# Optimization experiments

Hardware: AMD Instinct MI355X
Metric: run time of the kernel (lower is better)

The kernel has to match this reference:

```python
import jax, jax.numpy as jnp
import numpy as np

B, L, D, H = 2, 2048, 1024, 16
Dh = D // H

def setup_inputs() -> dict:
    key = jax.random.key(0)
    kx, kq, kk, kv, ko = jax.random.split(key, 5)
    scale = 1.0 / np.sqrt(D)
    return {
        "x": jax.random.normal(kx, (B, L, D), dtype=jnp.float32),
        "Wq": jax.random.normal(kq, (D, H, Dh), dtype=jnp.float32) * scale,
        "Wk": jax.random.normal(kk, (D, H, Dh), dtype=jnp.float32) * scale,
        "Wv": jax.random.normal(kv, (D, H, Dh), dtype=jnp.float32) * scale,
        "Wout": jax.random.normal(ko, (H, Dh, D), dtype=jnp.float32) * (1.0 / np.sqrt(D)),
    }

def reference(x, Wq, Wk, Wv, Wout):
    # QKV projections: [B,L,D] x [D,H,Dh] -> [B,L,H,Dh]
    q = jnp.einsum('bld,dhe->blhe', x, Wq)
    k = jnp.einsum('bld,dhe->blhe', x, Wk)
    v = jnp.einsum('bld,dhe->blhe', x, Wv)
    # scores [B,H,L,L]
    a = jnp.einsum('bqhd,bkhd->bhqk', q, k) / (Dh ** 0.5)
    Lq = x.shape[1]
    mask = jnp.tril(jnp.ones((1, 1, Lq, Lq), dtype=jnp.bool_))
    NEG_INF = jnp.finfo(jnp.float32).min
    a = jnp.where(mask, a, NEG_INF)
    a = jax.nn.softmax(a, axis=-1)
    o = jnp.einsum('bhqk,bkhd->bqhd', a, v)
    # output projection: [B,L,H,Dh] x [H,Dh,D] -> [B,L,D]
    return jnp.einsum('blhe,hed->bld', o, Wout)
```

## Files before the change

kernel.cpp:

```cpp
#include <hip/hip_runtime.h>

typedef __bf16 bf16x8 __attribute__((ext_vector_type(8)));
typedef __bf16 bf16x4 __attribute__((ext_vector_type(4)));
typedef float  floatx4 __attribute__((ext_vector_type(4)));
typedef float  floatx16 __attribute__((ext_vector_type(16)));

constexpr int Bc = 2, Lc = 2048, Dc = 1024, Hc = 16, Dhc = 64;
constexpr int Mr = 4096;

__device__ __forceinline__ void gl_lds16(const void* g, void* l) {
  __builtin_amdgcn_global_load_lds(
      (const __attribute__((address_space(1))) void*)g,
      (__attribute__((address_space(3))) void*)l, 16, 0, 0);
}

__global__ __launch_bounds__(256) void k_pack(const float* __restrict__ X,
                                              const float* __restrict__ W0,
                                              const float* __restrict__ W1,
                                              const float* __restrict__ W2,
                                              const float* __restrict__ W3,
                                              __bf16* __restrict__ Pw,
                                              __bf16* __restrict__ Px) {
  __shared__ __align__(16) __bf16 tile[64][66];
  int bid = blockIdx.x;
  int t = threadIdx.x;
  if (bid < 1024) {
    int z = bid >> 8, rem = bid & 255;
    int k0 = (rem & 15) << 6, n0 = (rem >> 4) << 6;
    const float* W = (z == 0) ? W0 : (z == 1) ? W1 : (z == 2) ? W2 : W3;
    __bf16* P = Pw + (size_t)z * 1024 * 1024;
    int r = t >> 2, cc = t & 3;
    const float4* src = (const float4*)&W[(size_t)(k0 + r) * 1024 + n0 + cc * 16];
#pragma unroll
    for (int i = 0; i < 4; i++) {
      float4 v = src[i];
      tile[r][cc * 16 + i * 4 + 0] = (__bf16)v.x;
      tile[r][cc * 16 + i * 4 + 1] = (__bf16)v.y;
      tile[r][cc * 16 + i * 4 + 2] = (__bf16)v.z;
      tile[r][cc * 16 + i * 4 + 3] = (__bf16)v.w;
    }
    __syncthreads();
#pragma unroll
    for (int i = 0; i < 2; i++) {
      int c = t + i * 256;
      int pl = c >> 6, nl = c & 63;
      bf16x8 o;
#pragma unroll
      for (int j = 0; j < 8; j++) o[j] = tile[pl * 8 + j][nl];
      *(bf16x8*)&P[((size_t)(k0 / 8 + pl) * 1024 + n0 + nl) * 8] = o;
    }
  } else {
    int xid = bid - 1024;
    int m0 = (xid & 63) << 6, p0 = (xid >> 6) << 2;
    int r = t >> 2, cc = t & 3;
    const float4* src = (const float4*)&X[(size_t)(m0 + r) * 1024 + p0 * 8 + cc * 8];
    float4 v0 = src[0], v1 = src[1];
    bf16x8 o;
    o[0] = (__bf16)v0.x; o[1] = (__bf16)v0.y; o[2] = (__bf16)v0.z; o[3] = (__bf16)v0.w;
    o[4] = (__bf16)v1.x; o[5] = (__bf16)v1.y; o[6] = (__bf16)v1.z; o[7] = (__bf16)v1.w;
    *(bf16x8*)&tile[0][r * 32 + cc * 8] = o;
    __syncthreads();
    int pc = t >> 6, ml = t & 63;
    bf16x8 q = *(bf16x8*)&tile[0][ml * 32 + pc * 8];
    *(bf16x8*)&Px[((size_t)(p0 + pc) * Mr + m0 + ml) * 8] = q;
  }
}

__global__ __launch_bounds__(256) void k_gemm_qkv(const __bf16* __restrict__ Ap8,
                                                  const __bf16* __restrict__ Bp8,
                                                  __bf16* __restrict__ Qb,
                                                  __bf16* __restrict__ Kb,
                                                  __bf16* __restrict__ Vb) {
  constexpr int KCB = 2080;
  constexpr int HB = 4 * KCB;
  __shared__ __align__(16) char smem[4 * HB];
  int t = threadIdx.x, lane = t & 63, w = t >> 6;
  int lh = lane >> 5, l32 = lane & 31;
  int m0 = blockIdx.x * 128;
  int mat = blockIdx.y >> 3;
  const __bf16* Bbase = Bp8 + (size_t)mat * 1024 * 1024;
  int n0loc = (blockIdx.y & 7) * 128;
  int wm = (w & 1) * 64, wn = (w >> 1) * 64;
  floatx16 acc[2][2] = {};

  auto issue = [&](int it, char* buf) {
    int kp = it << 2;
    const __bf16* ga = Ap8 + ((size_t)(kp + w) * Mr + m0 + lane) * 8;
    const __bf16* gb = Bbase + ((size_t)(kp + w) * 1024 + n0loc + lane) * 8;
    char* la = buf + w * KCB;
    char* lb = buf + HB + w * KCB;
    gl_lds16(ga, la);
    gl_lds16(ga + 512, la + 1024);
    gl_lds16(gb, lb);
    gl_lds16(gb + 512, lb + 1024);
  };

  issue(0, smem);
  for (int it = 0; it < 32; it++) {
    char* cur = smem + (it & 1) * (2 * HB);
    char* nxt = smem + ((it & 1) ^ 1) * (2 * HB);
    __syncthreads();
    if (it < 31) issue(it + 1, nxt);
    bf16x8 af[2][2], bfv[2][2];
#pragma unroll
    for (int s = 0; s < 2; s++) {
#pragma unroll
      for (int mt = 0; mt < 2; mt++)
        af[s][mt] = *(const bf16x8*)(cur + (2 * s + lh) * KCB + (wm + mt * 32 + l32) * 16);
#pragma unroll
      for (int nt = 0; nt < 2; nt++)
        bfv[s][nt] = *(const bf16x8*)(cur + HB + (2 * s + lh) * KCB + (wn + nt * 32 + l32) * 16);
    }
#pragma unroll
    for (int s = 0; s < 2; s++)
#pragma unroll
      for (int mt = 0; mt < 2; mt++)
#pragma unroll
        for (int nt = 0; nt < 2; nt++)
          acc[mt][nt] = __builtin_amdgcn_mfma_f32_32x32x16_bf16(af[s][mt], bfv[s][nt], acc[mt][nt], 0, 0, 0);
  }

  __syncthreads();

  __bf16* sl = (__bf16*)(smem + w * HB);
  int b = (m0 + wm) >> 11;
  int lbase = (m0 + wm) & 2047;
  int h = (n0loc + wn) >> 6;
  int bh2 = b * 16 + h;
  __bf16* dst;
  float scl = 1.0f;
  if (mat == 0) {
    dst = Qb + (((size_t)(bh2 * 64 + (lbase >> 5)) * 4) << 9);
    scl = 0.18033688011112042f;
  } else if (mat == 1) {
    dst = Kb + (((size_t)(bh2 * 32 + (lbase >> 6)) * 8) << 9);
  } else {
    dst = Vb + (((size_t)(bh2 * 32 + (lbase >> 6)) * 8) << 9);
  }
#pragma unroll
  for (int mt = 0; mt < 2; mt++)
#pragma unroll
    for (int nt = 0; nt < 2; nt++)
#pragma unroll
      for (int reg = 0; reg < 16; reg++) {
        int l_loc = mt * 32 + (reg & 3) + ((reg >> 2) << 3) + (lh << 2);
        int e = nt * 32 + l32;
        int off;
        if (mat == 0)
          off = ((l_loc >> 5) * 4 + ((l_loc >> 4) & 1) * 2 + (e >> 5)) * 512 +
                (((e >> 3) & 3) * 16 + (l_loc & 15)) * 8 + (e & 7);
        else if (mat == 1)
          off = ((l_loc >> 4) * 2 + (e >> 5)) * 512 +
                (((e >> 3) & 3) * 16 + (l_loc & 15)) * 8 + (e & 7);
        else
          off = ((e >> 4) * 2 + (l_loc >> 5)) * 512 +
                (((l_loc >> 2) & 3) * 16 + (e & 15)) * 8 + ((l_loc >> 4) & 1) * 4 + (l_loc & 3);
        sl[off] = (__bf16)(acc[mt][nt][reg] * scl);
      }
  __builtin_amdgcn_s_waitcnt(0);
#pragma unroll
  for (int i = 0; i < 8; i++) {
    int c = i * 64 + lane;
    bf16x8 v = *(bf16x8*)(sl + c * 8);
    *(bf16x8*)(dst + c * 8) = v;
  }
}

__global__ __launch_bounds__(256) void k_gemm_out(const __bf16* __restrict__ Ap8,
                                                  const __bf16* __restrict__ Bp8,
                                                  float* __restrict__ outF) {
  constexpr int KCB_A = 2080;
  constexpr int KCB_B = 1056;
  constexpr int BUF = 4 * KCB_A + 4 * KCB_B;
  __shared__ __align__(16) char smem[33792];
  int t = threadIdx.x, lane = t & 63, w = t >> 6;
  int lh = lane >> 5, l32 = lane & 31;
  int m0 = blockIdx.x * 128, n0 = blockIdx.y * 64;
  int wm = w * 32;
  floatx16 acc[2] = {};

  auto issue = [&](int it, char* buf) {
    int kp = it << 2;
    const __bf16* ga = Ap8 + ((size_t)(kp + w) * Mr + m0 + lane) * 8;
    const __bf16* gb = Bp8 + ((size_t)(kp + w) * 1024 + n0 + lane) * 8;
    char* la = buf + w * KCB_A;
    char* lb = buf + 4 * KCB_A + w * KCB_B;
    gl_lds16(ga, la);
    gl_lds16(ga + 512, la + 1024);
    gl_lds16(gb, lb);
  };

  issue(0, smem);
  for (int it = 0; it < 32; it++) {
    char* cur = smem + (it & 1) * BUF;
    char* nxt = smem + ((it & 1) ^ 1) * BUF;
    __syncthreads();
    if (it < 31) issue(it + 1, nxt);
    bf16x8 af[2], bfv[2][2];
#pragma unroll
    for (int s = 0; s < 2; s++) {
      af[s] = *(const bf16x8*)(cur + (2 * s + lh) * KCB_A + (wm + l32) * 16);
#pragma unroll
      for (int nt = 0; nt < 2; nt++)
        bfv[s][nt] = *(const bf16x8*)(cur + 4 * KCB_A + (2 * s + lh) * KCB_B + (nt * 32 + l32) * 16);
    }
#pragma unroll
    for (int s = 0; s < 2; s++)
#pragma unroll
      for (int nt = 0; nt < 2; nt++)
        acc[nt] = __builtin_amdgcn_mfma_f32_32x32x16_bf16(af[s], bfv[s][nt], acc[nt], 0, 0, 0);
  }

  __syncthreads();
  float* slf = (float*)(smem + w * 8448);
#pragma unroll
  for (int nt = 0; nt < 2; nt++)
#pragma unroll
    for (int reg = 0; reg < 16; reg++) {
      int rrow = (reg & 3) + ((reg >> 2) << 3) + (lh << 2);
      slf[rrow * 66 + nt * 32 + l32] = acc[nt][reg];
    }
  __builtin_amdgcn_s_waitcnt(0);
#pragma unroll
  for (int i = 0; i < 8; i++) {
    int c = i * 64 + lane;
    int row = c >> 4, sub = c & 15;
    float4 v = *(float4*)(slf + row * 66 + sub * 4);
    *(float4*)&outF[(size_t)(m0 + wm + row) * 1024 + n0 + sub * 4] = v;
  }
}

__global__ __launch_bounds__(256) void k_attn(const __bf16* __restrict__ Qf,
                                              const __bf16* __restrict__ Kf,
                                              const __bf16* __restrict__ Vf,
                                              __bf16* __restrict__ Op8) {
  __shared__ __align__(16) __bf16 POt[4][32][72];
  __shared__ float Pl[4][2][16];
  int t = threadIdx.x;
  int lane = t & 63, w = t >> 6;
  int quad = lane >> 4, l16 = lane & 15;
  int bid = blockIdx.x;
  int xcd = bid & 7, g = bid >> 3;
  int bh = xcd * 4 + (g & 3);
  int qt = 63 - (g >> 2);
  int qbase = qt * 32;

  const __bf16* Qp = Qf + (((size_t)(bh * 64 + qt) * 4) << 9) + lane * 8;
  bf16x8 qf[2][2];
#pragma unroll
  for (int mi = 0; mi < 2; mi++)
#pragma unroll
    for (int kk = 0; kk < 2; kk++)
      qf[mi][kk] = *(const bf16x8*)(Qp + ((mi * 2 + kk) << 9));

  floatx4 ot[4][2] = {};
  float l_s[2] = {0.f, 0.f};

  auto do_tile = [&](int kt, bool domask) {
    int kbase = kt * 64;
    const __bf16* Kp = Kf + (((size_t)(bh * 32 + kt) * 8) << 9) + lane * 8;
    const __bf16* Vp = Vf + (((size_t)(bh * 32 + kt) * 8) << 9) + lane * 8;
    bf16x8 ka[4][2], va[4][2];
#pragma unroll
    for (int kb = 0; kb < 4; kb++)
#pragma unroll
      for (int kk = 0; kk < 2; kk++) {
        ka[kb][kk] = *(const bf16x8*)(Kp + ((kb * 2 + kk) << 9));
        va[kb][kk] = *(const bf16x8*)(Vp + ((kb * 2 + kk) << 9));
      }

    floatx4 st[4][2] = {};
#pragma unroll
    for (int kb = 0; kb < 4; kb++)
#pragma unroll
      for (int mi = 0; mi < 2; mi++) {
        st[kb][mi] = __builtin_amdgcn_mfma_f32_16x16x32_bf16(ka[kb][0], qf[mi][0], st[kb][mi], 0, 0, 0);
        st[kb][mi] = __builtin_amdgcn_mfma_f32_16x16x32_bf16(ka[kb][1], qf[mi][1], st[kb][mi], 0, 0, 0);
      }

    bf16x8 pb[2][2];
#pragma unroll
    for (int mi = 0; mi < 2; mi++) {
      int q_g = qbase + mi * 16 + l16;
      float pv[4][4];
      float psum = 0.f;
#pragma unroll
      for (int kb = 0; kb < 4; kb++)
#pragma unroll
        for (int r = 0; r < 4; r++) {
          float v = st[kb][mi][r];
          if (domask) {
            int key = kbase + kb * 16 + quad * 4 + r;
            if (key > q_g) v = -__builtin_inff();
          }
          float p = __builtin_amdgcn_exp2f(v);
          pv[kb][r] = p;
          psum += p;
        }
      l_s[mi] += psum;
#pragma unroll
      for (int kp = 0; kp < 2; kp++) {
        bf16x8 p8;
#pragma unroll
        for (int j = 0; j < 4; j++) {
          p8[j] = (__bf16)pv[kp * 2][j];
          p8[j + 4] = (__bf16)pv[kp * 2 + 1][j];
        }
        pb[mi][kp] = p8;
      }
    }

#pragma unroll
    for (int kbd = 0; kbd < 4; kbd++)
#pragma unroll
      for (int mi = 0; mi < 2; mi++) {
        ot[kbd][mi] = __builtin_amdgcn_mfma_f32_16x16x32_bf16(va[kbd][0], pb[mi][0], ot[kbd][mi], 0, 0, 0);
        ot[kbd][mi] = __builtin_amdgcn_mfma_f32_16x16x32_bf16(va[kbd][1], pb[mi][1], ot[kbd][mi], 0, 0, 0);
      }
  };

  int nkt = ((qt * 32 + 31) >> 6) + 1;
  for (int kt = w; kt < nkt - 1; kt += 4) do_tile(kt, false);
  if (((nkt - 1) & 3) == w) do_tile(nkt - 1, true);

#pragma unroll
  for (int mi = 0; mi < 2; mi++) {
    l_s[mi] += __shfl_xor(l_s[mi], 16);
    l_s[mi] += __shfl_xor(l_s[mi], 32);
  }

#pragma unroll
  for (int mi = 0; mi < 2; mi++) {
    if (quad == 0) Pl[w][mi][l16] = l_s[mi];
#pragma unroll
    for (int kbd = 0; kbd < 4; kbd++) {
      bf16x4 p4;
#pragma unroll
      for (int r = 0; r < 4; r++) p4[r] = (__bf16)ot[kbd][mi][r];
      *(bf16x4*)&POt[w][mi * 16 + l16][kbd * 16 + quad * 4] = p4;
    }
  }
  __syncthreads();

  int oct = lane >> 3, rl = lane & 7;
  int ql = w * 8 + rl;
  float lstar = 0.f;
#pragma unroll
  for (int ww = 0; ww < 4; ww++) lstar += Pl[ww][ql >> 4][ql & 15];
  float inv = 1.f / lstar;
  float accv[8] = {};
#pragma unroll
  for (int ww = 0; ww < 4; ww++) {
    bf16x8 pv8 = *(const bf16x8*)&POt[ww][ql][oct * 8];
#pragma unroll
    for (int j = 0; j < 8; j++) accv[j] += (float)pv8[j];
  }
  bf16x8 ov;
#pragma unroll
  for (int j = 0; j < 8; j++) ov[j] = (__bf16)(accv[j] * inv);
  int b = bh >> 4, h = bh & 15;
  size_t row = (size_t)b * Lc + qbase + ql;
  *(bf16x8*)&Op8[((size_t)(h * 8 + oct) * Mr + row) * 8] = ov;
}

extern "C" void kernel_launch(void* const* d_in, const int* in_sizes, int n_in,
                              void* d_out, int out_size, void* d_ws, size_t ws_size,
                              hipStream_t stream) {
  const float* x  = (const float*)d_in[0];
  const float* Wq = (const float*)d_in[1];
  const float* Wk = (const float*)d_in[2];
  const float* Wv = (const float*)d_in[3];
  const float* Wo = (const float*)d_in[4];
  float* out = (float*)d_out;

  if (ws_size < (size_t)50331648) return;
  __bf16* xb   = (__bf16*)d_ws;
  __bf16* wqkv = xb + (size_t)Mr * Dc;
  __bf16* wot  = wqkv + (size_t)3 * Dc * Dc;
  __bf16* Qfr  = wot + (size_t)Dc * Dc;
  __bf16* Kfr  = Qfr + (size_t)Mr * Dc;
  __bf16* Vfr  = Kfr + (size_t)Mr * Dc;
  __bf16* Op8  = Vfr + (size_t)Mr * Dc;

  k_pack<<<3072, 256, 0, stream>>>(x, Wq, Wk, Wv, Wo, wqkv, xb);

  k_gemm_qkv<<<dim3(32, 24), 256, 0, stream>>>(xb, wqkv, Qfr, Kfr, Vfr);

  k_attn<<<dim3(2048), 256, 0, stream>>>(Qfr, Kfr, Vfr, Op8);

  k_gemm_out<<<dim3(32, 16), 256, 0, stream>>>(Op8, wot, out);
}
```

Measured before the change: 159.0 us.

## Triple-buffer LDS in QKV and output GEMMs with partial vmcnt waits

Switches the QKV and output-projection GEMM main loops from double to triple buffering. Two K-stages are prefetched ahead, and an explicit s_waitcnt vmcnt(N) waits only for the oldest stage before a raw barrier. This replaces the full __syncthreads wait on all outstanding loads. The aim is to hide more global-to-LDS latency, at the cost of 50% more LDS per block, which may lower occupancy.

Result: no change. 161.3 us (+1.4%).

```diff
diff --git a/kernel.cpp b/kernel.cpp
--- a/kernel.cpp
+++ b/kernel.cpp
@@ -73,7 +73,8 @@
                                                   __bf16* __restrict__ Vb) {
   constexpr int KCB = 2080;
   constexpr int HB = 4 * KCB;
-  __shared__ __align__(16) char smem[4 * HB];
+  constexpr int STG = 2 * HB;
+  __shared__ __align__(16) char smem[3 * STG];
   int t = threadIdx.x, lane = t & 63, w = t >> 6;
   int lh = lane >> 5, l32 = lane & 31;
   int m0 = blockIdx.x * 128;
@@ -96,11 +97,19 @@
   };
 
   issue(0, smem);
+  issue(1, smem + STG);
+  int cs = 0;
   for (int it = 0; it < 32; it++) {
-    char* cur = smem + (it & 1) * (2 * HB);
-    char* nxt = smem + ((it & 1) ^ 1) * (2 * HB);
-    __syncthreads();
-    if (it < 31) issue(it + 1, nxt);
+    char* cur = smem + cs * STG;
+    if (it < 31)
+      asm volatile("s_waitcnt vmcnt(4) lgkmcnt(0)" ::: "memory");
+    else
+      asm volatile("s_waitcnt vmcnt(0) lgkmcnt(0)" ::: "memory");
+    __builtin_amdgcn_s_barrier();
+    if (it < 30) {
+      int ns = cs - 1; if (ns < 0) ns += 3;
+      issue(it + 2, smem + ns * STG);
+    }
     bf16x8 af[2][2], bfv[2][2];
 #pragma unroll
     for (int s = 0; s < 2; s++) {
@@ -118,6 +127,7 @@
 #pragma unroll
         for (int nt = 0; nt < 2; nt++)
           acc[mt][nt] = __builtin_amdgcn_mfma_f32_32x32x16_bf16(af[s][mt], bfv[s][nt], acc[mt][nt], 0, 0, 0);
+    cs = (cs == 2) ? 0 : cs + 1;
   }
 
   __syncthreads();
@@ -171,8 +181,8 @@
                                                   float* __restrict__ outF) {
   constexpr int KCB_A = 2080;
   constexpr int KCB_B = 1056;
-  constexpr int BUF = 4 * KCB_A + 4 * KCB_B;
-  __shared__ __align__(16) char smem[33792];
+  constexpr int STG = 4 * KCB_A + 4 * KCB_B;
+  __shared__ __align__(16) char smem[3 * STG];
   int t = threadIdx.x, lane = t & 63, w = t >> 6;
   int lh = lane >> 5, l32 = lane & 31;
   int m0 = blockIdx.x * 128, n0 = blockIdx.y * 64;
@@ -191,11 +201,19 @@
   };
 
   issue(0, smem);
+  issue(1, smem + STG);
+  int cs = 0;
   for (int it = 0; it < 32; it++) {
-    char* cur = smem + (it & 1) * BUF;
-    char* nxt = smem + ((it & 1) ^ 1) * BUF;
-    __syncthreads();
-    if (it < 31) issue(it + 1, nxt);
+    char* cur = smem + cs * STG;
+    if (it < 31)
+      asm volatile("s_waitcnt vmcnt(3) lgkmcnt(0)" ::: "memory");
+    else
+      asm volatile("s_waitcnt vmcnt(0) lgkmcnt(0)" ::: "memory");
+    __builtin_amdgcn_s_barrier();
+    if (it < 30) {
+      int ns = cs - 1; if (ns < 0) ns += 3;
+      issue(it + 2, smem + ns * STG);
+    }
     bf16x8 af[2], bfv[2][2];
 #pragma unroll
     for (int s = 0; s < 2; s++) {
@@ -209,6 +227,7 @@
 #pragma unroll
       for (int nt = 0; nt < 2; nt++)
         acc[nt] = __builtin_amdgcn_mfma_f32_32x32x16_bf16(af[s], bfv[s][nt], acc[nt], 0, 0, 0);
+    cs = (cs == 2) ? 0 : cs + 1;
   }
 
   __syncthreads();
```
